# Optimization experiments

Hardware: AMD Instinct MI355X
Metric: run time of the kernel (lower is better)

Reference implementation:

```python
import jax, jax.numpy as jnp
import numpy as np

N_NODES = 100000
N_EDGES = 3200000
EPS = 1e-5


def gcn_conv(x, edge_index, W, b):
    # PyG GCNConv: sym-normalized A+I, transform-then-propagate
    h = x @ W                                   # [N, out]
    src, dst = edge_index[0], edge_index[1]
    ones = jnp.ones(edge_index.shape[1], dtype=x.dtype)
    deg = jax.ops.segment_sum(ones, dst, num_segments=N_NODES) + 1.0  # +1 self-loop
    dis = jax.lax.rsqrt(deg)                    # deg^{-1/2}
    coef = (dis[src] * dis[dst])[:, None]
    agg = jax.ops.segment_sum(h[src] * coef, dst, num_segments=N_NODES)
    agg = agg + h * (dis * dis)[:, None]        # self-loop contribution
    return agg + b


def batch_norm(x, gamma, beta):
    mu = jnp.mean(x, axis=0)
    var = jnp.mean(jnp.square(x - mu), axis=0)
    return (x - mu) * jax.lax.rsqrt(var + EPS) * gamma + beta


def setup_inputs() -> dict:
    key = jax.random.key(0)
    ks = jax.random.split(key, 12)
    d = {
        "x": jax.random.normal(ks[0], (N_NODES, 256), dtype=jnp.float32),
        "edge_index": jax.random.randint(ks[1], (2, N_EDGES), 0, N_NODES, dtype=jnp.int32),
        "W1": jax.random.normal(ks[2], (256, 128), dtype=jnp.float32) * (1.0 / np.sqrt(256)),
        "b1": jnp.zeros((128,), jnp.float32),
        "g1": jnp.ones((128,), jnp.float32),
        "bt1": jnp.zeros((128,), jnp.float32),
        "W2": jax.random.normal(ks[3], (128, 64), dtype=jnp.float32) * (1.0 / np.sqrt(128)),
        "b2": jnp.zeros((64,), jnp.float32),
        "g2": jnp.ones((64,), jnp.float32),
        "bt2": jnp.zeros((64,), jnp.float32),
        "W3": jax.random.normal(ks[4], (64, 32), dtype=jnp.float32) * (1.0 / np.sqrt(64)),
        "b3": jnp.zeros((32,), jnp.float32),
        "g3": jnp.ones((32,), jnp.float32),
        "bt3": jnp.zeros((32,), jnp.float32),
        "Wfc": jax.random.normal(ks[5], (32, 1), dtype=jnp.float32) * (1.0 / np.sqrt(32)),
        "bfc": jnp.zeros((1,), jnp.float32),
    }
    return d


def reference(x, edge_index, W1, b1, g1, bt1, W2, b2, g2, bt2, W3, b3, g3, bt3, Wfc, bfc):
    h = jax.nn.relu(batch_norm(gcn_conv(x, edge_index, W1, b1), g1, bt1))
    h = jax.nn.relu(batch_norm(gcn_conv(h, edge_index, W2, b2), g2, bt2))
    h = jax.nn.relu(batch_norm(gcn_conv(h, edge_index, W3, b3), g3, bt3))
    return h @ Wfc + bfc
```

## Files before the change

### kernel.cpp

```cpp
#include <hip/hip_runtime.h>
#include <hip/hip_fp16.h>

#define EPS 1e-5f
constexpr int NT = 256;
constexpr int BSH = 9;
constexpr int BNODES = 1 << BSH;
constexpr int CH = 4096;

typedef _Float16 v8h __attribute__((ext_vector_type(8)));
typedef float v4f __attribute__((ext_vector_type(4)));


__global__ __launch_bounds__(NT) void bhist_kernel(const int* __restrict__ dst, int* __restrict__ gbhist,
                                                   int E, int NBUK) {
    __shared__ int h[512];
    int tid = threadIdx.x;
    for (int i = tid; i < 512; i += NT) h[i] = 0;
    __syncthreads();
    for (int e = blockIdx.x * NT + tid; e < E; e += gridDim.x * NT)
        atomicAdd(&h[dst[e] >> BSH], 1);
    __syncthreads();
    for (int i = tid; i < NBUK; i += NT)
        if (h[i]) atomicAdd(&gbhist[i], h[i]);
}


__global__ __launch_bounds__(NT) void bscan_kernel(const int* __restrict__ gbhist, int* __restrict__ bbase,
                                                   int* __restrict__ gcur, int E, int NBUK) {
    __shared__ int wsum[5];
    int tid = threadIdx.x;
    int lane = tid & 63, wid = tid >> 6;
    int e0 = (2 * tid < NBUK) ? gbhist[2 * tid] : 0;
    int e1 = (2 * tid + 1 < NBUK) ? gbhist[2 * tid + 1] : 0;
    int u = e0 + e1;
    int incl = u;
    #pragma unroll
    for (int off = 1; off < 64; off <<= 1) {
        int t = __shfl_up(incl, off, 64);
        if (lane >= off) incl += t;
    }
    if (lane == 63) wsum[wid] = incl;
    __syncthreads();
    if (tid == 0) { int s = 0; for (int w = 0; w < 4; w++) { int t = wsum[w]; wsum[w] = s; s += t; } }
    __syncthreads();
    int base = wsum[wid] + incl - u;
    if (2 * tid < NBUK)     { bbase[2 * tid] = base;          gcur[2 * tid] = base; }
    if (2 * tid + 1 < NBUK) { bbase[2 * tid + 1] = base + e0; gcur[2 * tid + 1] = base + e0; }
    if (tid == 0) bbase[NBUK] = E;
}


__global__ __launch_bounds__(NT) void part_kernel(const int* __restrict__ src, const int* __restrict__ dst,
                                                  int* __restrict__ gcur, int* __restrict__ ebuf,
                                                  int E, int NBUK) {
    constexpr int EPT = CH / NT;
    __shared__ int hist[512];
    __shared__ int lscan[512];
    __shared__ int gbase[512];
    __shared__ int2 stage[CH];
    int tid = threadIdx.x;
    int lane = tid & 63;
    int e0 = blockIdx.x * CH;

    for (int i = tid; i < 512; i += NT) hist[i] = 0;
    __syncthreads();

    int2 ed[EPT]; int rank[EPT]; int buk[EPT];
    #pragma unroll
    for (int j = 0; j < EPT; j++) {
        int e = e0 + j * NT + tid;
        if (e < E) {
            ed[j].x = src[e]; ed[j].y = dst[e];
            buk[j] = ed[j].y >> BSH;
            rank[j] = atomicAdd(&hist[buk[j]], 1);
        } else buk[j] = -1;
    }
    __syncthreads();
    if (tid < 64) {
        int bi = tid * 8;
        int v[8]; int s = 0;
        #pragma unroll
        for (int j = 0; j < 8; j++) { v[j] = s; s += hist[bi + j]; }
        int incl = s;
        #pragma unroll
        for (int off = 1; off < 64; off <<= 1) {
            int t = __shfl_up(incl, off, 64);
            if (lane >= off) incl += t;
        }
        int lb = incl - s;
        #pragma unroll
        for (int j = 0; j < 8; j++) lscan[bi + j] = lb + v[j];
    }
    __syncthreads();
    for (int i = tid; i < NBUK; i += NT) {
        int c = hist[i];
        gbase[i] = c ? atomicAdd(&gcur[i], c) : 0;
    }
    #pragma unroll
    for (int j = 0; j < EPT; j++)
        if (buk[j] >= 0) stage[lscan[buk[j]] + rank[j]] = ed[j];
    __syncthreads();
    int cnt = min(E - e0, CH);
    for (int i = tid; i < cnt; i += NT) {
        int2 e = stage[i];
        int b = e.y >> BSH;
        ebuf[gbase[b] + (i - lscan[b])] = ((e.y & (BNODES - 1)) << 18) | e.x;
    }
}


__global__ __launch_bounds__(NT) void bfill_kernel(const int* __restrict__ ebuf, const int* __restrict__ bbase,
                                                   int* __restrict__ row_start,
                                                   float* __restrict__ dis, int* __restrict__ csr, int N) {
    __shared__ int ldeg[BNODES];
    __shared__ int lrs[BNODES];
    __shared__ int wsum[5];
    int tid = threadIdx.x;
    int lane = tid & 63, wid = tid >> 6;
    int b = blockIdx.x;
    int node0 = b << BSH;
    int nn = min(BNODES, N - node0);
    int beg = bbase[b], end = bbase[b + 1];

    for (int i = tid; i < BNODES; i += NT) ldeg[i] = 0;
    __syncthreads();
    for (int i = beg + tid; i < end; i += NT)
        atomicAdd(&ldeg[ebuf[i] >> 18], 1);
    __syncthreads();
    int e0 = ldeg[2 * tid], e1 = ldeg[2 * tid + 1];
    int u = e0 + e1;
    int incl = u;
    #pragma unroll
    for (int off = 1; off < 64; off <<= 1) {
        int t = __shfl_up(incl, off, 64);
        if (lane >= off) incl += t;
    }
    if (lane == 63) wsum[wid] = incl;
    __syncthreads();
    if (tid == 0) { int s = 0; for (int w = 0; w < 4; w++) { int t = wsum[w]; wsum[w] = s; s += t; } }
    __syncthreads();
    int base = wsum[wid] + incl - u;
    lrs[2 * tid] = base;
    lrs[2 * tid + 1] = base + e0;
    __syncthreads();
    for (int i = tid; i < nn; i += NT) {
        int dg = ldeg[i];
        row_start[node0 + i] = beg + lrs[i];
        dis[node0 + i] = rsqrtf((float)dg + 1.0f);
    }
    if (b == gridDim.x - 1 && tid == 0) row_start[N] = end;
    __syncthreads();
    for (int i = tid; i < BNODES; i += NT) ldeg[i] = 0;
    __syncthreads();
    for (int i = beg + tid; i < end; i += NT) {
        int code = ebuf[i];
        int l = code >> 18;
        int off = atomicAdd(&ldeg[l], 1);
        csr[beg + lrs[l] + off] = code & 0x3FFFF;
    }
}


__global__ __launch_bounds__(NT) void prepw_kernel(const float* __restrict__ W1, const float* __restrict__ W2,
                                                   const float* __restrict__ W3, __half* __restrict__ Wt1,
                                                   __half* __restrict__ Wt2, __half* __restrict__ Wt3) {
    int i = blockIdx.x * NT + threadIdx.x;
    if (i < 256 * 128) {
        int k = i >> 7, f = i & 127;
        Wt1[f * 256 + k] = __float2half(W1[i]);
    } else if (i < 256 * 128 + 128 * 64) {
        int j = i - 256 * 128; int k = j >> 6, f = j & 63;
        Wt2[f * 128 + k] = __float2half(W2[j]);
    } else if (i < 256 * 128 + 128 * 64 + 64 * 32) {
        int j = i - 256 * 128 - 128 * 64; int k = j >> 5, f = j & 31;
        Wt3[f * 64 + k] = __float2half(W3[j]);
    }
}


template<int K, int F, bool NORM>
__global__ __launch_bounds__(NT) void mgemm_kernel(const void* __restrict__ Xv, const __half* __restrict__ Wt,
                                                   const float* __restrict__ dis, const float* __restrict__ an,
                                                   const float* __restrict__ cn, __half* __restrict__ out, int N) {
    constexpr int KC = 32;
    constexpr int CG = F / 16;
    constexpr int LDA = KC + 8;
    constexpr int ASZ = NORM ? K : 1;
    __shared__ __half As[64 * LDA];
    __shared__ __half Bs[F * LDA];
    __shared__ float as_[ASZ], cs_[ASZ];

    int tid = threadIdx.x;
    if constexpr (NORM) {
        for (int i = tid; i < K; i += NT) { as_[i] = an[i]; cs_[i] = cn[i]; }
        __syncthreads();
    }
    int row0 = blockIdx.x * 64;
    int wid = tid >> 6, lane = tid & 63;
    int quad = lane >> 4, l16 = lane & 15;
    int tr = tid >> 3;
    int tk = (tid & 7) * 4;

    v4f acc[CG];
    #pragma unroll
    for (int g = 0; g < CG; g++) acc[g] = (v4f)0.f;

    for (int k0 = 0; k0 < K; k0 += KC) {
        #pragma unroll
        for (int r = tr; r < 64; r += 32) {
            int row = row0 + r;
            __half h0, h1, h2, h3;
            if (row < N) {
                if constexpr (NORM) {
                    const __half2* xp = (const __half2*)((const __half*)Xv + (size_t)row * K + k0 + tk);
                    float2 v0 = __half22float2(xp[0]);
                    float2 v1 = __half22float2(xp[1]);
                    h0 = __float2half(fmaxf(v0.x * as_[k0 + tk]     + cs_[k0 + tk],     0.f));
                    h1 = __float2half(fmaxf(v0.y * as_[k0 + tk + 1] + cs_[k0 + tk + 1], 0.f));
                    h2 = __float2half(fmaxf(v1.x * as_[k0 + tk + 2] + cs_[k0 + tk + 2], 0.f));
                    h3 = __float2half(fmaxf(v1.y * as_[k0 + tk + 3] + cs_[k0 + tk + 3], 0.f));
                } else {
                    float4 v = *(const float4*)((const float*)Xv + (size_t)row * K + k0 + tk);
                    h0 = __float2half(v.x); h1 = __float2half(v.y);
                    h2 = __float2half(v.z); h3 = __float2half(v.w);
                }
            } else {
                h0 = h1 = h2 = h3 = __float2half(0.f);
            }
            __half2* dst = (__half2*)&As[r * LDA + tk];
            dst[0] = __halves2half2(h0, h1);
            dst[1] = __halves2half2(h2, h3);
        }
        #pragma unroll
        for (int n = tr; n < F; n += 32) {
            const __half2* wp = (const __half2*)(Wt + (size_t)n * K + k0 + tk);
            __half2* dst = (__half2*)&Bs[n * LDA + tk];
            dst[0] = wp[0];
            dst[1] = wp[1];
        }
        __syncthreads();
        v8h a = *(const v8h*)&As[(wid * 16 + l16) * LDA + quad * 8];
        #pragma unroll
        for (int g = 0; g < CG; g++) {
            v8h b = *(const v8h*)&Bs[(g * 16 + l16) * LDA + quad * 8];
            acc[g] = __builtin_amdgcn_mfma_f32_16x16x32_f16(a, b, acc[g], 0, 0, 0);
        }
        __syncthreads();
    }
    #pragma unroll
    for (int reg = 0; reg < 4; reg++) {
        int row = row0 + wid * 16 + quad * 4 + reg;
        if (row < N) {
            float d = dis[row];
            #pragma unroll
            for (int g = 0; g < CG; g++)
                out[(size_t)row * F + g * 16 + l16] = __float2half(d * acc[g][reg]);
        }
    }
}


template<int F, int U>
__global__ __launch_bounds__(NT) void agg_kernel(const __half* __restrict__ hd, const int* __restrict__ csr,
                                                 const int* __restrict__ row_start,
                                                 const float* __restrict__ dis, const float* __restrict__ b,
                                                 __half* __restrict__ pre, int N) {
    constexpr int LR = F / 8;
    constexpr int SUBS = 64 / LR;
    constexpr int FSH = (F == 128) ? 7 : (F == 64) ? 6 : 5;
    int node = (blockIdx.x * NT + threadIdx.x) >> 6;
    int lane = threadIdx.x & 63;
    int fl = lane % LR, sub = lane / LR;
    if (node >= N) return;
    int beg = row_start[node];
    int cnt = row_start[node + 1] - beg;
    int fo = fl * 8;

    __half2 hacc[U][4];
    #pragma unroll
    for (int u = 0; u < U; u++)
        #pragma unroll
        for (int j = 0; j < 4; j++) hacc[u][j] = __halves2half2(__half(0.f), __half(0.f));

    int i = 0;
    for (; i + SUBS * U <= cnt; i += SUBS * U) {
        int s[U];
        #pragma unroll
        for (int u = 0; u < U; u++) s[u] = csr[beg + i + u * SUBS + sub];
        #pragma unroll
        for (int u = 0; u < U; u++) {
            int4 v = *(const int4*)(hd + ((s[u] << FSH) + fo));
            const __half2* hv = (const __half2*)&v;
            #pragma unroll
            for (int j = 0; j < 4; j++) hacc[u][j] = hacc[u][j] + hv[j];
        }
    }
    for (; i + sub < cnt; i += SUBS) {
        int s = csr[beg + i + sub];
        int4 v = *(const int4*)(hd + ((s << FSH) + fo));
        const __half2* hv = (const __half2*)&v;
        #pragma unroll
        for (int j = 0; j < 4; j++) hacc[0][j] = hacc[0][j] + hv[j];
    }
    if (sub == 0) {
        int4 v = *(const int4*)(hd + ((node << FSH) + fo));
        const __half2* hv = (const __half2*)&v;
        #pragma unroll
        for (int j = 0; j < 4; j++) hacc[0][j] = hacc[0][j] + hv[j];
    }
    float acc[8];
    #pragma unroll
    for (int j = 0; j < 4; j++) {
        float2 f = __half22float2(hacc[0][j]);
        acc[2 * j] = f.x; acc[2 * j + 1] = f.y;
    }
    #pragma unroll
    for (int u = 1; u < U; u++)
        #pragma unroll
        for (int j = 0; j < 4; j++) {
            float2 f = __half22float2(hacc[u][j]);
            acc[2 * j] += f.x; acc[2 * j + 1] += f.y;
        }
    #pragma unroll
    for (int m = LR; m < 64; m <<= 1)
        #pragma unroll
        for (int j = 0; j < 8; j++) acc[j] += __shfl_xor(acc[j], m, 64);
    if (sub == 0) {
        float d = dis[node];
        float4 b0 = *(const float4*)(b + fo);
        float4 b1 = *(const float4*)(b + fo + 4);
        __half2 h[4];
        h[0] = __floats2half2_rn(d * acc[0] + b0.x, d * acc[1] + b0.y);
        h[1] = __floats2half2_rn(d * acc[2] + b0.z, d * acc[3] + b0.w);
        h[2] = __floats2half2_rn(d * acc[4] + b1.x, d * acc[5] + b1.y);
        h[3] = __floats2half2_rn(d * acc[6] + b1.z, d * acc[7] + b1.w);
        *(int4*)(pre + ((node << FSH) + fo)) = *(int4*)h;
    }
}


template<int F>
__global__ __launch_bounds__(NT) void stats_kernel(const __half* __restrict__ pre, float* __restrict__ S1,
                                                   float* __restrict__ S2, int N) {
    constexpr int FP = F / 2;
    constexpr int RPB = NT / FP;
    int tid = threadIdx.x;
    int f = tid % FP, r0 = tid / FP;
    float s1x = 0.f, s1y = 0.f, s2x = 0.f, s2y = 0.f;
    const __half2* p2 = (const __half2*)pre;
    for (int node = blockIdx.x * RPB + r0; node < N; node += gridDim.x * RPB) {
        float2 v = __half22float2(p2[(size_t)node * FP + f]);
        s1x += v.x; s1y += v.y; s2x += v.x * v.x; s2y += v.y * v.y;
    }
    __shared__ float l1x[NT], l1y[NT], l2x[NT], l2y[NT];
    l1x[tid] = s1x; l1y[tid] = s1y; l2x[tid] = s2x; l2y[tid] = s2y;
    __syncthreads();
    if (tid < FP) {
        #pragma unroll
        for (int j = 1; j < RPB; j++) {
            s1x += l1x[tid + j * FP]; s1y += l1y[tid + j * FP];
            s2x += l2x[tid + j * FP]; s2y += l2y[tid + j * FP];
        }
        atomicAdd(&S1[2 * tid], s1x); atomicAdd(&S1[2 * tid + 1], s1y);
        atomicAdd(&S2[2 * tid], s2x); atomicAdd(&S2[2 * tid + 1], s2y);
    }
}

__global__ void params_kernel(const float* __restrict__ S1, const float* __restrict__ S2,
                              const float* __restrict__ g, const float* __restrict__ bt,
                              float* __restrict__ a, float* __restrict__ c, int N, int F) {
    int f = threadIdx.x;
    if (f < F) {
        float inv = 1.0f / (float)N;
        float mu = S1[f] * inv;
        float var = fmaxf(S2[f] * inv - mu * mu, 0.f);
        float av = g[f] * rsqrtf(var + EPS);
        a[f] = av;
        c[f] = bt[f] - mu * av;
    }
}


__global__ __launch_bounds__(NT) void fc_kernel(const __half* __restrict__ pre, const float* __restrict__ a,
                                                const float* __restrict__ c, const float* __restrict__ wfc,
                                                const float* __restrict__ bfc, float* __restrict__ out, int N) {
    __shared__ float wa[32], wc[32], ww[32];
    int tid = threadIdx.x;
    if (tid < 32) { wa[tid] = a[tid]; wc[tid] = c[tid]; ww[tid] = wfc[tid]; }
    __syncthreads();
    int n = blockIdx.x * NT + tid;
    if (n >= N) return;
    const __half2* p = (const __half2*)(pre + (size_t)n * 32);
    float acc = bfc[0];
    #pragma unroll
    for (int i = 0; i < 16; i++) {
        float2 v = __half22float2(p[i]);
        int f = i * 2;
        acc += fmaxf(v.x * wa[f] + wc[f], 0.f) * ww[f];
        acc += fmaxf(v.y * wa[f + 1] + wc[f + 1], 0.f) * ww[f + 1];
    }
    out[n] = acc;
}


extern "C" void kernel_launch(void* const* d_in, const int* in_sizes, int n_in,
                              void* d_out, int out_size, void* d_ws, size_t ws_size,
                              hipStream_t stream) {
    const float* x   = (const float*)d_in[0];
    const int*   ei  = (const int*)d_in[1];
    const float* W1  = (const float*)d_in[2];
    const float* b1  = (const float*)d_in[3];
    const float* g1  = (const float*)d_in[4];
    const float* bt1 = (const float*)d_in[5];
    const float* W2  = (const float*)d_in[6];
    const float* b2  = (const float*)d_in[7];
    const float* g2  = (const float*)d_in[8];
    const float* bt2 = (const float*)d_in[9];
    const float* W3  = (const float*)d_in[10];
    const float* b3  = (const float*)d_in[11];
    const float* g3  = (const float*)d_in[12];
    const float* bt3 = (const float*)d_in[13];
    const float* Wfc = (const float*)d_in[14];
    const float* bfc = (const float*)d_in[15];
    float* out = (float*)d_out;

    int N = in_sizes[0] / 256;
    int E = in_sizes[1] / 2;
    const int* src = ei;
    const int* dst = ei + E;
    int NBUK = (N + BNODES - 1) >> BSH;

    char* ws = (char*)d_ws;
    size_t off = 0;
    auto alloc = [&](size_t bytes) -> char* {
        char* p = ws + off;
        off += (bytes + 255) & ~(size_t)255;
        return p;
    };
    __half* bufA     = (__half*)alloc((size_t)N * 128 * 2);
    __half* bufB     = (__half*)alloc((size_t)N * 128 * 2);
    int*   ebuf      = (int*)alloc((size_t)E * 4);
    int*   csr       = (int*)alloc((size_t)E * 4);
    int*   row_start = (int*)alloc((size_t)(N + 1) * 4);
    float* dis       = (float*)alloc((size_t)N * 4);
    int*   gbhist    = (int*)alloc((size_t)NBUK * 4);
    int*   bbase     = (int*)alloc((size_t)(NBUK + 1) * 4);
    int*   gcur      = (int*)alloc((size_t)NBUK * 4);
    __half* Wt1      = (__half*)alloc(256 * 128 * 2);
    __half* Wt2      = (__half*)alloc(128 * 64 * 2);
    __half* Wt3      = (__half*)alloc(64 * 32 * 2);
    float* stats = (float*)alloc(448 * 4 * 2);
    float* S1_1 = stats;       float* S2_1 = S1_1 + 128;
    float* S1_2 = S2_1 + 128;  float* S2_2 = S1_2 + 64;
    float* S1_3 = S2_2 + 64;   float* S2_3 = S1_3 + 32;
    float* a1 = S2_3 + 32; float* c1 = a1 + 128;
    float* a2 = c1 + 128;  float* c2 = a2 + 64;
    float* a3 = c2 + 64;   float* c3 = a3 + 32;

    hipMemsetAsync(gbhist, 0, (size_t)NBUK * 4, stream);
    hipMemsetAsync(stats, 0, 448 * 4, stream);

    bhist_kernel<<<512, NT, 0, stream>>>(dst, gbhist, E, NBUK);
    bscan_kernel<<<1, NT, 0, stream>>>(gbhist, bbase, gcur, E, NBUK);
    part_kernel<<<(E + CH - 1) / CH, NT, 0, stream>>>(src, dst, gcur, ebuf, E, NBUK);
    bfill_kernel<<<NBUK, NT, 0, stream>>>(ebuf, bbase, row_start, dis, csr, N);
    prepw_kernel<<<(256 * 128 + 128 * 64 + 64 * 32 + NT - 1) / NT, NT, 0, stream>>>(W1, W2, W3, Wt1, Wt2, Wt3);

    int GB = (N + 63) / 64;
    int AB = (N + 3) / 4;
    int NB = (N + NT - 1) / NT;
    mgemm_kernel<256, 128, false><<<GB, NT, 0, stream>>>(x, Wt1, dis, nullptr, nullptr, bufA, N);
    agg_kernel<128, 4><<<AB, NT, 0, stream>>>(bufA, csr, row_start, dis, b1, bufB, N);
    stats_kernel<128><<<256, NT, 0, stream>>>(bufB, S1_1, S2_1, N);
    params_kernel<<<1, 128, 0, stream>>>(S1_1, S2_1, g1, bt1, a1, c1, N, 128);
    mgemm_kernel<128, 64, true><<<GB, NT, 0, stream>>>(bufB, Wt2, dis, a1, c1, bufA, N);
    agg_kernel<64, 2><<<AB, NT, 0, stream>>>(bufA, csr, row_start, dis, b2, bufB, N);
    stats_kernel<64><<<256, NT, 0, stream>>>(bufB, S1_2, S2_2, N);
    params_kernel<<<1, 64, 0, stream>>>(S1_2, S2_2, g2, bt2, a2, c2, N, 64);
    mgemm_kernel<64, 32, true><<<GB, NT, 0, stream>>>(bufB, Wt3, dis, a2, c2, bufA, N);
    agg_kernel<32, 1><<<AB, NT, 0, stream>>>(bufA, csr, row_start, dis, b3, bufB, N);
    stats_kernel<32><<<256, NT, 0, stream>>>(bufB, S1_3, S2_3, N);
    params_kernel<<<1, 32, 0, stream>>>(S1_3, S2_3, g3, bt3, a3, c3, N, 32);
    fc_kernel<<<NB, NT, 0, stream>>>(bufB, a3, c3, Wfc, bfc, out, N);
}
```

Baseline: 623.1 us.

## Fuse graph build with first GEMM, pad CSR rows, fold BN params into consumers

Merges the edge-partition and CSR-fill kernels with slices of the first-layer GEMM into two combined kernels, so graph construction and the X@W1 transform run concurrently. CSR rows are padded to multiples of 16 using a dummy zero node, which removes the tail loop in aggregation. For layer 1 the source-side degree scaling moves from the GEMM epilogue into aggregation through a half-precision dis array. The separate params kernels are removed and BN scale/shift is recomputed inside the GEMM and FC kernels. In exchange the code does more gather traffic on padding entries and adds extra half-precision rounding.

```diff
diff --git a/kernel.cpp b/kernel.cpp
--- a/kernel.cpp
+++ b/kernel.cpp
@@ -6,6 +6,7 @@
 constexpr int BSH = 9;
 constexpr int BNODES = 1 << BSH;
 constexpr int CH = 4096;
+constexpr int PADCAP = 15 * BNODES;
 
 typedef _Float16 v8h __attribute__((ext_vector_type(8)));
 typedef float v4f __attribute__((ext_vector_type(4)));
@@ -50,17 +51,17 @@
 }
 
 
-__global__ __launch_bounds__(NT) void part_kernel(const int* __restrict__ src, const int* __restrict__ dst,
-                                                  int* __restrict__ gcur, int* __restrict__ ebuf,
-                                                  int E, int NBUK) {
+__device__ __forceinline__ void part_body(int bx, const int* __restrict__ src, const int* __restrict__ dst,
+                                          int* __restrict__ gcur, int* __restrict__ ebuf,
+                                          int E, int NBUK, char* smem) {
     constexpr int EPT = CH / NT;
-    __shared__ int hist[512];
-    __shared__ int lscan[512];
-    __shared__ int gbase[512];
-    __shared__ int2 stage[CH];
+    int* hist  = (int*)smem;
+    int* lscan = hist + 512;
+    int* gbase = lscan + 512;
+    int2* stage = (int2*)(gbase + 512);
     int tid = threadIdx.x;
     int lane = tid & 63;
-    int e0 = blockIdx.x * CH;
+    int e0 = bx * CH;
 
     for (int i = tid; i < 512; i += NT) hist[i] = 0;
     __syncthreads();
@@ -109,18 +110,20 @@
 }
 
 
-__global__ __launch_bounds__(NT) void bfill_kernel(const int* __restrict__ ebuf, const int* __restrict__ bbase,
-                                                   int* __restrict__ row_start,
-                                                   float* __restrict__ dis, int* __restrict__ csr, int N) {
-    __shared__ int ldeg[BNODES];
-    __shared__ int lrs[BNODES];
-    __shared__ int wsum[5];
+__device__ __forceinline__ void bfill_body(int bx, const int* __restrict__ ebuf, const int* __restrict__ bbase,
+                                           int* __restrict__ row_start, int* __restrict__ pdeg,
+                                           float* __restrict__ dis, __half* __restrict__ dis_h,
+                                           int* __restrict__ csr, int N, char* smem) {
+    int* ldeg = (int*)smem;
+    int* lrs  = ldeg + 512;
+    int* wsum = lrs + 512;
     int tid = threadIdx.x;
     int lane = tid & 63, wid = tid >> 6;
-    int b = blockIdx.x;
+    int b = bx;
     int node0 = b << BSH;
     int nn = min(BNODES, N - node0);
     int beg = bbase[b], end = bbase[b + 1];
+    int begp = beg + b * PADCAP;
 
     for (int i = tid; i < BNODES; i += NT) ldeg[i] = 0;
     __syncthreads();
@@ -128,7 +131,8 @@
         atomicAdd(&ldeg[ebuf[i] >> 18], 1);
     __syncthreads();
     int e0 = ldeg[2 * tid], e1 = ldeg[2 * tid + 1];
-    int u = e0 + e1;
+    int p0 = (e0 + 15) & ~15, p1 = (e1 + 15) & ~15;
+    int u = p0 + p1;
     int incl = u;
     #pragma unroll
     for (int off = 1; off < 64; off <<= 1) {
@@ -141,14 +145,17 @@
     __syncthreads();
     int base = wsum[wid] + incl - u;
     lrs[2 * tid] = base;
-    lrs[2 * tid + 1] = base + e0;
+    lrs[2 * tid + 1] = base + p0;
     __syncthreads();
     for (int i = tid; i < nn; i += NT) {
         int dg = ldeg[i];
-        row_start[node0 + i] = beg + lrs[i];
-        dis[node0 + i] = rsqrtf((float)dg + 1.0f);
-    }
-    if (b == gridDim.x - 1 && tid == 0) row_start[N] = end;
+        pdeg[node0 + i] = (dg + 15) & ~15;
+        row_start[node0 + i] = begp + lrs[i];
+        float dv = rsqrtf((float)dg + 1.0f);
+        dis[node0 + i] = dv;
+        dis_h[node0 + i] = __float2half(dv);
+    }
+    if (bx == 0 && tid == 0) dis_h[N] = __float2half(0.f);
     __syncthreads();
     for (int i = tid; i < BNODES; i += NT) ldeg[i] = 0;
     __syncthreads();
@@ -156,14 +163,22 @@
         int code = ebuf[i];
         int l = code >> 18;
         int off = atomicAdd(&ldeg[l], 1);
-        csr[beg + lrs[l] + off] = code & 0x3FFFF;
+        csr[begp + lrs[l] + off] = code & 0x3FFFF;
+    }
+    __syncthreads();
+    for (int i = tid; i < nn; i += NT) {
+        int dg = ldeg[i];
+        int pd = (dg + 15) & ~15;
+        int cbase = begp + lrs[i];
+        for (int k = dg; k < pd; k++) csr[cbase + k] = N;
     }
 }
 
 
 __global__ __launch_bounds__(NT) void prepw_kernel(const float* __restrict__ W1, const float* __restrict__ W2,
                                                    const float* __restrict__ W3, __half* __restrict__ Wt1,
-                                                   __half* __restrict__ Wt2, __half* __restrict__ Wt3) {
+                                                   __half* __restrict__ Wt2, __half* __restrict__ Wt3,
+                                                   __half* __restrict__ bufA, int N) {
     int i = blockIdx.x * NT + threadIdx.x;
     if (i < 256 * 128) {
         int k = i >> 7, f = i & 127;
@@ -174,28 +189,39 @@
     } else if (i < 256 * 128 + 128 * 64 + 64 * 32) {
         int j = i - 256 * 128 - 128 * 64; int k = j >> 5, f = j & 31;
         Wt3[f * 64 + k] = __float2half(W3[j]);
-    }
-}
-
-
-template<int K, int F, bool NORM>
-__global__ __launch_bounds__(NT) void mgemm_kernel(const void* __restrict__ Xv, const __half* __restrict__ Wt,
-                                                   const float* __restrict__ dis, const float* __restrict__ an,
-                                                   const float* __restrict__ cn, __half* __restrict__ out, int N) {
+    } else if (i < 256 * 128 + 128 * 64 + 64 * 32 + 128) {
+        bufA[(size_t)N * 128 + (i - (256 * 128 + 128 * 64 + 64 * 32))] = __float2half(0.f);
+    }
+}
+
+
+template<int K, int F, bool NORM, bool SC>
+__device__ __forceinline__ void mgemm_body(int bx, const void* __restrict__ Xv, const __half* __restrict__ Wt,
+                                           const float* __restrict__ dis, const float* __restrict__ S1,
+                                           const float* __restrict__ S2, const float* __restrict__ g,
+                                           const float* __restrict__ bt, __half* __restrict__ out, int N,
+                                           char* smem) {
     constexpr int KC = 32;
     constexpr int CG = F / 16;
     constexpr int LDA = KC + 8;
-    constexpr int ASZ = NORM ? K : 1;
-    __shared__ __half As[64 * LDA];
-    __shared__ __half Bs[F * LDA];
-    __shared__ float as_[ASZ], cs_[ASZ];
+    __half* As = (__half*)smem;
+    __half* Bs = (__half*)(smem + 64 * LDA * 2);
+    float* as_ = (float*)(smem + 64 * LDA * 2 + F * LDA * 2);
+    float* cs_ = as_ + K;
 
     int tid = threadIdx.x;
     if constexpr (NORM) {
-        for (int i = tid; i < K; i += NT) { as_[i] = an[i]; cs_[i] = cn[i]; }
+        float inv = 1.0f / (float)N;
+        for (int i = tid; i < K; i += NT) {
+            float mu = S1[i] * inv;
+            float var = fmaxf(S2[i] * inv - mu * mu, 0.f);
+            float av = g[i] * rsqrtf(var + EPS);
+            as_[i] = av;
+            cs_[i] = bt[i] - mu * av;
+        }
         __syncthreads();
     }
-    int row0 = blockIdx.x * 64;
+    int row0 = bx * 64;
     int wid = tid >> 6, lane = tid & 63;
     int quad = lane >> 4, l16 = lane & 15;
     int tr = tid >> 3;
@@ -203,7 +229,7 @@
 
     v4f acc[CG];
     #pragma unroll
-    for (int g = 0; g < CG; g++) acc[g] = (v4f)0.f;
+    for (int gg = 0; gg < CG; gg++) acc[gg] = (v4f)0.f;
 
     for (int k0 = 0; k0 < K; k0 += KC) {
         #pragma unroll
@@ -241,9 +267,9 @@
         __syncthreads();
         v8h a = *(const v8h*)&As[(wid * 16 + l16) * LDA + quad * 8];
         #pragma unroll
-        for (int g = 0; g < CG; g++) {
-            v8h b = *(const v8h*)&Bs[(g * 16 + l16) * LDA + quad * 8];
-            acc[g] = __builtin_amdgcn_mfma_f32_16x16x32_f16(a, b, acc[g], 0, 0, 0);
+        for (int gg = 0; gg < CG; gg++) {
+            v8h b = *(const v8h*)&Bs[(gg * 16 + l16) * LDA + quad * 8];
+            acc[gg] = __builtin_amdgcn_mfma_f32_16x16x32_f16(a, b, acc[gg], 0, 0, 0);
         }
         __syncthreads();
     }
@@ -251,62 +277,109 @@
     for (int reg = 0; reg < 4; reg++) {
         int row = row0 + wid * 16 + quad * 4 + reg;
         if (row < N) {
-            float d = dis[row];
+            float d = SC ? dis[row] : 1.0f;
             #pragma unroll
-            for (int g = 0; g < CG; g++)
-                out[(size_t)row * F + g * 16 + l16] = __float2half(d * acc[g][reg]);
-        }
-    }
-}
-
-
-template<int F, int U>
+            for (int gg = 0; gg < CG; gg++)
+                out[(size_t)row * F + gg * 16 + l16] = __float2half(d * acc[gg][reg]);
+        } else if (row == N) {
+            #pragma unroll
+            for (int gg = 0; gg < CG; gg++)
+                out[(size_t)row * F + gg * 16 + l16] = __float2half(0.f);
+        }
+    }
+}
+
+template<int K, int F, bool NORM, bool SC>
+__global__ __launch_bounds__(NT) void mgemm_kernel(const void* __restrict__ Xv, const __half* __restrict__ Wt,
+                                                   const float* __restrict__ dis, const float* __restrict__ S1,
+                                                   const float* __restrict__ S2, const float* __restrict__ g,
+                                                   const float* __restrict__ bt, __half* __restrict__ out, int N) {
+    constexpr int SMB = 64 * 40 * 2 + F * 40 * 2 + (NORM ? 8 * K : 0);
+    __shared__ __align__(16) char smem[SMB];
+    mgemm_body<K, F, NORM, SC>(blockIdx.x, Xv, Wt, dis, S1, S2, g, bt, out, N, smem);
+}
+
+
+__global__ __launch_bounds__(NT) void fat1_kernel(const int* __restrict__ src, const int* __restrict__ dst,
+                                                  int* __restrict__ gcur, int* __restrict__ ebuf, int E, int NBUK,
+                                                  int PB, const float* __restrict__ x, const __half* __restrict__ Wt1,
+                                                  __half* __restrict__ bufA, int N) {
+    __shared__ __align__(16) char smem[38912];
+    if ((int)blockIdx.x < PB)
+        part_body(blockIdx.x, src, dst, gcur, ebuf, E, NBUK, smem);
+    else
+        mgemm_body<256, 128, false, false>((int)blockIdx.x - PB, x, Wt1, nullptr, nullptr, nullptr, nullptr,
+                                           nullptr, bufA, N, smem);
+}
+
+__global__ __launch_bounds__(NT) void fat2_kernel(const int* __restrict__ ebuf, const int* __restrict__ bbase,
+                                                  int* __restrict__ row_start, int* __restrict__ pdeg,
+                                                  float* __restrict__ dis, __half* __restrict__ dis_h,
+                                                  int* __restrict__ csr, const float* __restrict__ x,
+                                                  const __half* __restrict__ Wt1, __half* __restrict__ bufA,
+                                                  int N, int NBUK, int A) {
+    __shared__ __align__(16) char smem[15872];
+    if ((int)blockIdx.x < NBUK)
+        bfill_body(blockIdx.x, ebuf, bbase, row_start, pdeg, dis, dis_h, csr, N, smem);
+    else
+        mgemm_body<256, 128, false, false>((int)blockIdx.x - NBUK + A, x, Wt1, nullptr, nullptr, nullptr, nullptr,
+                                           nullptr, bufA, N, smem);
+}
+
+
+template<int F, int U, bool DISW>
 __global__ __launch_bounds__(NT) void agg_kernel(const __half* __restrict__ hd, const int* __restrict__ csr,
-                                                 const int* __restrict__ row_start,
-                                                 const float* __restrict__ dis, const float* __restrict__ b,
-                                                 __half* __restrict__ pre, int N) {
+                                                 const int* __restrict__ row_start, const int* __restrict__ pdeg,
+                                                 const __half* __restrict__ dis_h, const float* __restrict__ dis,
+                                                 const float* __restrict__ b, __half* __restrict__ pre, int N) {
     constexpr int LR = F / 8;
     constexpr int SUBS = 64 / LR;
     constexpr int FSH = (F == 128) ? 7 : (F == 64) ? 6 : 5;
     int node = (blockIdx.x * NT + threadIdx.x) >> 6;
+    if (node >= N) return;
     int lane = threadIdx.x & 63;
     int fl = lane % LR, sub = lane / LR;
-    if (node >= N) return;
     int beg = row_start[node];
-    int cnt = row_start[node + 1] - beg;
+    int iters = pdeg[node] >> 4;
     int fo = fl * 8;
 
     __half2 hacc[U][4];
     #pragma unroll
     for (int u = 0; u < U; u++)
         #pragma unroll
-        for (int j = 0; j < 4; j++) hacc[u][j] = __halves2half2(__half(0.f), __half(0.f));
-
-    int i = 0;
-    for (; i + SUBS * U <= cnt; i += SUBS * U) {
+        for (int j = 0; j < 4; j++) hacc[u][j] = __half2half2(__half(0.f));
+
+    if (sub == 0) {
+        int4 v = *(const int4*)(hd + (((size_t)node << FSH) + fo));
+        const __half2* hv = (const __half2*)&v;
+        if constexpr (DISW) {
+            __half2 dd = __half2half2(dis_h[node]);
+            #pragma unroll
+            for (int j = 0; j < 4; j++) hacc[0][j] = __hmul2(hv[j], dd);
+        } else {
+            #pragma unroll
+            for (int j = 0; j < 4; j++) hacc[0][j] = hv[j];
+        }
+    }
+    const int* cp = csr + beg + sub;
+    for (int it = 0; it < iters; ++it) {
         int s[U];
         #pragma unroll
-        for (int u = 0; u < U; u++) s[u] = csr[beg + i + u * SUBS + sub];
+        for (int u = 0; u < U; u++) s[u] = cp[u * SUBS];
+        cp += 16;
         #pragma unroll
         for (int u = 0; u < U; u++) {
-            int4 v = *(const int4*)(hd + ((s[u] << FSH) + fo));
+            int4 v = *(const int4*)(hd + (((size_t)s[u] << FSH) + fo));
             const __half2* hv = (const __half2*)&v;
-            #pragma unroll
-            for (int j = 0; j < 4; j++) hacc[u][j] = hacc[u][j] + hv[j];
-        }
-    }
-    for (; i + sub < cnt; i += SUBS) {
-        int s = csr[beg + i + sub];
-        int4 v = *(const int4*)(hd + ((s << FSH) + fo));
-        const __half2* hv = (const __half2*)&v;
-        #pragma unroll
-        for (int j = 0; j < 4; j++) hacc[0][j] = hacc[0][j] + hv[j];
-    }
-    if (sub == 0) {
-        int4 v = *(const int4*)(hd + ((node << FSH) + fo));
-        const __half2* hv = (const __half2*)&v;
-        #pragma unroll
-        for (int j = 0; j < 4; j++) hacc[0][j] = hacc[0][j] + hv[j];
+            if constexpr (DISW) {
+                __half2 dd = __half2half2(dis_h[s[u]]);
+                #pragma unroll
+                for (int j = 0; j < 4; j++) hacc[u][j] = __hfma2(hv[j], dd, hacc[u][j]);
+            } else {
+                #pragma unroll
+                for (int j = 0; j < 4; j++) hacc[u][j] = __hadd2(hacc[u][j], hv[j]);
+            }
+        }
     }
     float acc[8];
     #pragma unroll
@@ -334,7 +407,7 @@
         h[1] = __floats2half2_rn(d * acc[2] + b0.z, d * acc[3] + b0.w);
         h[2] = __floats2half2_rn(d * acc[4] + b1.x, d * acc[5] + b1.y);
         h[3] = __floats2half2_rn(d * acc[6] + b1.z, d * acc[7] + b1.w);
-        *(int4*)(pre + ((node << FSH) + fo)) = *(int4*)h;
+        *(int4*)(pre + (((size_t)node << FSH) + fo)) = *(int4*)h;
     }
 }
 
@@ -366,27 +439,20 @@
     }
 }
 
-__global__ void params_kernel(const float* __restrict__ S1, const float* __restrict__ S2,
-                              const float* __restrict__ g, const float* __restrict__ bt,
-                              float* __restrict__ a, float* __restrict__ c, int N, int F) {
-    int f = threadIdx.x;
-    if (f < F) {
-        float inv = 1.0f / (float)N;
-        float mu = S1[f] * inv;
-        float var = fmaxf(S2[f] * inv - mu * mu, 0.f);
-        float av = g[f] * rsqrtf(var + EPS);
-        a[f] = av;
-        c[f] = bt[f] - mu * av;
-    }
-}
-
-
-__global__ __launch_bounds__(NT) void fc_kernel(const __half* __restrict__ pre, const float* __restrict__ a,
-                                                const float* __restrict__ c, const float* __restrict__ wfc,
+
+__global__ __launch_bounds__(NT) void fc_kernel(const __half* __restrict__ pre, const float* __restrict__ S1,
+                                                const float* __restrict__ S2, const float* __restrict__ g,
+                                                const float* __restrict__ bt, const float* __restrict__ wfc,
                                                 const float* __restrict__ bfc, float* __restrict__ out, int N) {
     __shared__ float wa[32], wc[32], ww[32];
     int tid = threadIdx.x;
-    if (tid < 32) { wa[tid] = a[tid]; wc[tid] = c[tid]; ww[tid] = wfc[tid]; }
+    if (tid < 32) {
+        float inv = 1.0f / (float)N;
+        float mu = S1[tid] * inv;
+        float var = fmaxf(S2[tid] * inv - mu * mu, 0.f);
+        float av = g[tid] * rsqrtf(var + EPS);
+        wa[tid] = av; wc[tid] = bt[tid] - mu * av; ww[tid] = wfc[tid];
+    }
     __syncthreads();
     int n = blockIdx.x * NT + tid;
     if (n >= N) return;
@@ -437,49 +503,48 @@
         off += (bytes + 255) & ~(size_t)255;
         return p;
     };
-    __half* bufA     = (__half*)alloc((size_t)N * 128 * 2);
+    __half* bufA     = (__half*)alloc((size_t)(N + 1) * 128 * 2);
     __half* bufB     = (__half*)alloc((size_t)N * 128 * 2);
     int*   ebuf      = (int*)alloc((size_t)E * 4);
-    int*   csr       = (int*)alloc((size_t)E * 4);
-    int*   row_start = (int*)alloc((size_t)(N + 1) * 4);
+    int*   csr       = (int*)alloc(((size_t)E + (size_t)NBUK * PADCAP) * 4);
+    int*   row_start = (int*)alloc((size_t)N * 4);
+    int*   pdeg      = (int*)alloc((size_t)N * 4);
     float* dis       = (float*)alloc((size_t)N * 4);
+    __half* dis_h    = (__half*)alloc((size_t)(N + 1) * 2);
     int*   gbhist    = (int*)alloc((size_t)NBUK * 4);
     int*   bbase     = (int*)alloc((size_t)(NBUK + 1) * 4);
     int*   gcur      = (int*)alloc((size_t)NBUK * 4);
     __half* Wt1      = (__half*)alloc(256 * 128 * 2);
     __half* Wt2      = (__half*)alloc(128 * 64 * 2);
     __half* Wt3      = (__half*)alloc(64 * 32 * 2);
-    float* stats = (float*)alloc(448 * 4 * 2);
+    float* stats = (float*)alloc(448 * 4);
     float* S1_1 = stats;       float* S2_1 = S1_1 + 128;
     float* S1_2 = S2_1 + 128;  float* S2_2 = S1_2 + 64;
     float* S1_3 = S2_2 + 64;   float* S2_3 = S1_3 + 32;
-    float* a1 = S2_3 + 32; float* c1 = a1 + 128;
-    float* a2 = c1 + 128;  float* c2 = a2 + 64;
-    float* a3 = c2 + 64;   float* c3 = a3 + 32;
 
     hipMemsetAsync(gbhist, 0, (size_t)NBUK * 4, stream);
     hipMemsetAsync(stats, 0, 448 * 4, stream);
 
+    int GB = (N + 63) / 64;
+    int PB = (E + CH - 1) / CH;
+    int A = (GB * 3) / 5;
+    int AB = (N + 3) / 4;
+    int NB = (N + NT - 1) / NT;
+
+    prepw_kernel<<<(256 * 128 + 128 * 64 + 64 * 32 + 128 + NT - 1) / NT, NT, 0, stream>>>(
+        W1, W2, W3, Wt1, Wt2, Wt3, bufA, N);
     bhist_kernel<<<512, NT, 0, stream>>>(dst, gbhist, E, NBUK);
     bscan_kernel<<<1, NT, 0, stream>>>(gbhist, bbase, gcur, E, NBUK);
-    part_kernel<<<(E + CH - 1) / CH, NT, 0, stream>>>(src, dst, gcur, ebuf, E, NBUK);
-    bfill_kernel<<<NBUK, NT, 0, stream>>>(ebuf, bbase, row_start, dis, csr, N);
-    prepw_kernel<<<(256 * 128 + 128 * 64 + 64 * 32 + NT - 1) / NT, NT, 0, stream>>>(W1, W2, W3, Wt1, Wt2, Wt3);
-
-    int GB = (N + 63) / 64;
-    int AB = (N + 3) / 4;
-    int NB = (N + NT - 1) / NT;
-    mgemm_kernel<256, 128, false><<<GB, NT, 0, stream>>>(x, Wt1, dis, nullptr, nullptr, bufA, N);
-    agg_kernel<128, 4><<<AB, NT, 0, stream>>>(bufA, csr, row_start, dis, b1, bufB, N);
+    fat1_kernel<<<PB + A, NT, 0, stream>>>(src, dst, gcur, ebuf, E, NBUK, PB, x, Wt1, bufA, N);
+    fat2_kernel<<<NBUK + (GB - A), NT, 0, stream>>>(ebuf, bbase, row_start, pdeg, dis, dis_h, csr,
+                                                    x, Wt1, bufA, N, NBUK, A);
+    agg_kernel<128, 4, true><<<AB, NT, 0, stream>>>(bufA, csr, row_start, pdeg, dis_h, dis, b1, bufB, N);
     stats_kernel<128><<<256, NT, 0, stream>>>(bufB, S1_1, S2_1, N);
-    params_kernel<<<1, 128, 0, stream>>>(S1_1, S2_1, g1, bt1, a1, c1, N, 128);
-    mgemm_kernel<128, 64, true><<<GB, NT, 0, stream>>>(bufB, Wt2, dis, a1, c1, bufA, N);
-    agg_kernel<64, 2><<<AB, NT, 0, stream>>>(bufA, csr, row_start, dis, b2, bufB, N);
+    mgemm_kernel<128, 64, true, true><<<GB, NT, 0, stream>>>(bufB, Wt2, dis, S1_1, S2_1, g1, bt1, bufA, N);
+    agg_kernel<64, 2, false><<<AB, NT, 0, stream>>>(bufA, csr, row_start, pdeg, dis_h, dis, b2, bufB, N);
     stats_kernel<64><<<256, NT, 0, stream>>>(bufB, S1_2, S2_2, N);
-    params_kernel<<<1, 64, 0, stream>>>(S1_2, S2_2, g2, bt2, a2, c2, N, 64);
-    mgemm_kernel<64, 32, true><<<GB, NT, 0, stream>>>(bufB, Wt3, dis, a2, c2, bufA, N);
-    agg_kernel<32, 1><<<AB, NT, 0, stream>>>(bufA, csr, row_start, dis, b3, bufB, N);
+    mgemm_kernel<64, 32, true, true><<<GB, NT, 0, stream>>>(bufB, Wt3, dis, S1_2, S2_2, g2, bt2, bufA, N);
+    agg_kernel<32, 1, false><<<AB, NT, 0, stream>>>(bufA, csr, row_start, pdeg, dis_h, dis, b3, bufB, N);
     stats_kernel<32><<<256, NT, 0, stream>>>(bufB, S1_3, S2_3, N);
-    params_kernel<<<1, 32, 0, stream>>>(S1_3, S2_3, g3, bt3, a3, c3, N, 32);
-    fc_kernel<<<NB, NT, 0, stream>>>(bufB, a3, c3, Wfc, bfc, out, N);
-}
+    fc_kernel<<<NB, NT, 0, stream>>>(bufB, S1_3, S2_3, g3, bt3, Wfc, bfc, out, N);
+}
```

Result: faster. 604.3 us (-3.0%).
